# Kernel tuning notes

Hardware: AMD Instinct MI355X
Metric: run time of the kernel (lower is better)

## Reference

```python
import jax, jax.numpy as jnp
import numpy as np

B, H, W = 16, 512, 512
N_BINS = 511          # round(mean(shape)) - 1 for (512, 512)
MAX_R = 1.0           # (1 + min(shape)/max(shape)) / 2 for square image


def _bin_ids():
    # Precompute per-pixel radial shell index (replaces the list of boolean shell masks).
    frame = max(H, W)
    xx, yy = np.mgrid[:H, :W]
    ellipse = ((xx - H / 2) * 2 / frame) ** 2 + ((yy - W / 2) * 2 / frame) ** 2
    r2 = np.linspace(0.0, MAX_R, N_BINS + 1)[1:] ** 2
    # shell k = { r2[k-1] <= ellipse < r2[k] }; pixels with ellipse >= r2[-1] map to
    # overflow bin N_BINS and are dropped, exactly matching the xor'd ellipse masks.
    return jnp.asarray(np.searchsorted(r2, ellipse.ravel(), side='right').astype(np.int32))


BIN_IDS = _bin_ids()  # [H*W] int32 in [0, N_BINS]


def setup_inputs() -> dict:
    key = jax.random.key(0)
    k1, k2 = jax.random.split(key)
    return {
        "z_": jax.random.normal(k1, (B, H, W, 2), dtype=jnp.float32),
        "t_": jax.random.normal(k2, (B, H, W, 2), dtype=jnp.float32),
    }


def _shell_sums(x):
    # x: [B, H*W] -> per-shell sums [B, N_BINS+1] in a single fused segment-sum pass.
    return jax.vmap(lambda v: jax.ops.segment_sum(v, BIN_IDS, num_segments=N_BINS + 1))(x)


def reference(z_, t_):
    tc = t_[..., 0] + 1j * t_[..., 1]          # [B,H,W] complex target
    zc = z_[..., 0] + 1j * z_[..., 1]
    Ft = jnp.fft.fft2(tc, axes=(-2, -1))
    Fe = jnp.fft.fft2(zc - tc, axes=(-2, -1))
    norm_coeff = Ft.real ** 2 + Ft.imag ** 2   # |FFT(target)|^2, [B,H,W]
    errors = Fe.real ** 2 + Fe.imag ** 2       # |FFT(z - target)|^2
    es = _shell_sums(errors.reshape(B, -1))[:, :N_BINS]      # drop overflow bin
    ns = _shell_sums(norm_coeff.reshape(B, -1))[:, :N_BINS]
    nre = es / jnp.maximum(ns, 1e-8)           # per-batch, per-shell normed error
    # per_shell_loss = per-batch sum over shells; loss = mean over batch
    return jnp.mean(jnp.sum(nre, axis=1))
```

## Files before the change

kernel.cpp:

```cpp
#include <hip/hip_runtime.h>

#define HH 512
#define WW 512
#define NBATCH 16
#define NBINS 512

#define PI_F 3.14159265358979323846f

#define SW(r) ((r) ^ (((r) >> 4) & 0xF))
#define TSW(c, hh) (((c) << 3) + ((hh) ^ (((c) >> 1) & 7)))

__device__ __forceinline__ float2 cadd(float2 a, float2 b){ return make_float2(a.x+b.x, a.y+b.y); }
__device__ __forceinline__ float2 csub(float2 a, float2 b){ return make_float2(a.x-b.x, a.y-b.y); }
__device__ __forceinline__ float2 cmul(float2 a, float2 b){
    return make_float2(a.x*b.x - a.y*b.y, a.x*b.y + a.y*b.x);
}

__device__ __forceinline__ void dft8(const float2* a, float2* y) {
    const float s2 = 0.70710678118654752440f;
    float2 t02a = cadd(a[0], a[4]), t02s = csub(a[0], a[4]);
    float2 t13a = cadd(a[2], a[6]), t13s = csub(a[2], a[6]);
    float2 E0 = cadd(t02a, t13a);
    float2 E2 = csub(t02a, t13a);
    float2 E1 = make_float2(t02s.x + t13s.y, t02s.y - t13s.x);
    float2 E3 = make_float2(t02s.x - t13s.y, t02s.y + t13s.x);
    float2 u02a = cadd(a[1], a[5]), u02s = csub(a[1], a[5]);
    float2 u13a = cadd(a[3], a[7]), u13s = csub(a[3], a[7]);
    float2 O0 = cadd(u02a, u13a);
    float2 O2 = csub(u02a, u13a);
    float2 O1 = make_float2(u02s.x + u13s.y, u02s.y - u13s.x);
    float2 O3 = make_float2(u02s.x - u13s.y, u02s.y + u13s.x);
    float2 wO1 = make_float2(s2 * (O1.x + O1.y), s2 * (O1.y - O1.x));
    float2 wO2 = make_float2(O2.y, -O2.x);
    float2 wO3 = make_float2(s2 * (O3.y - O3.x), -s2 * (O3.x + O3.y));
    y[0] = cadd(E0, O0);  y[4] = csub(E0, O0);
    y[1] = cadd(E1, wO1); y[5] = csub(E1, wO1);
    y[2] = cadd(E2, wO2); y[6] = csub(E2, wO2);
    y[3] = cadd(E3, wO3); y[7] = csub(E3, wO3);
}

__device__ __forceinline__ void twiddle8(float base, float2* w) {
    float s1, c1, s4, c4;
    __sincosf(base, &s1, &c1);
    __sincosf(4.0f * base, &s4, &c4);
    w[0] = make_float2(1.0f, 0.0f);
    w[1] = make_float2(c1, s1);
    w[2] = cmul(w[1], w[1]);
    w[3] = cmul(w[2], w[1]);
    w[4] = make_float2(c4, s4);
    w[5] = cmul(w[4], w[1]);
    w[6] = cmul(w[4], w[2]);
    w[7] = cmul(w[4], w[3]);
}

__device__ __forceinline__ void fft512_stage0_store(float2* rb, int lane, const float2* a) {
    float2 y[8]; dft8(a, y);
    float2 w[8]; twiddle8(-PI_F * (float)lane * (1.0f / 256.0f), w);
#pragma unroll
    for (int r = 0; r < 8; ++r) rb[SW(8 * lane + r)] = cmul(y[r], w[r]);
}

__device__ __forceinline__ void fft512_stage1(float2* rb, int lane) {
    float2 a[8];
#pragma unroll
    for (int u = 0; u < 8; ++u) a[u] = rb[SW(lane + 64 * u)];
    float2 y[8]; dft8(a, y);
    float2 w[8]; twiddle8(-PI_F * (float)(lane >> 3) * (1.0f / 32.0f), w);
    const int qb = (lane & 7) + ((lane >> 3) << 6);
#pragma unroll
    for (int r = 0; r < 8; ++r) rb[SW(qb + 8 * r)] = cmul(y[r], w[r]);
}

__device__ __forceinline__ void fft512_stage2(const float2* rb, int lane, float2* y) {
    float2 a[8];
#pragma unroll
    for (int u = 0; u < 8; ++u) a[u] = rb[SW(lane + 64 * u)];
    dft8(a, y);
}

__global__ __launch_bounds__(512, 4)
void row_fft_kernel(const float2* __restrict__ z, const float2* __restrict__ t,
                    float2* __restrict__ fieldsT, int b0) {
    __shared__ float2 buf[8 * 512];
    const int tid  = threadIdx.x;
    const int lane = tid & 63;
    const int g    = tid >> 6;
    const int bid  = blockIdx.x;
    const int hg   = bid & 63;
    const int lb   = bid >> 6;
    const int b    = b0 + lb;
    const int h    = (hg << 3) | g;
    const size_t rowOff = ((size_t)(b * HH + h)) * WW;

    const float2* tr = t + rowOff;
    const float2* zr = z + rowOff;
    float2 tv[8], zv[8];
#pragma unroll
    for (int u = 0; u < 8; ++u) tv[u] = tr[lane + 64 * u];
#pragma unroll
    for (int u = 0; u < 8; ++u) zv[u] = zr[lane + 64 * u];

    float2* rb = buf + (g << 9);
#pragma unroll
    for (int f = 0; f < 2; ++f) {
        float2 a[8];
        if (f == 0) {
#pragma unroll
            for (int u = 0; u < 8; ++u) a[u] = tv[u];
        } else {
#pragma unroll
            for (int u = 0; u < 8; ++u) a[u] = make_float2(zv[u].x - tv[u].x,
                                                           zv[u].y - tv[u].y);
        }
        fft512_stage0_store(rb, lane, a);
        __builtin_amdgcn_wave_barrier();
        fft512_stage1(rb, lane);
        __builtin_amdgcn_wave_barrier();
        float2 y[8];
        fft512_stage2(rb, lane, y);

        __syncthreads();
#pragma unroll
        for (int r = 0; r < 8; ++r) {
            int c = lane + (r << 6);
            buf[TSW(c, g)] = y[r];
        }
        __syncthreads();
        float2* outF = fieldsT + ((size_t)(lb * 2 + f) << 18);
#pragma unroll
        for (int k = 0; k < 8; ++k) {
            int e  = tid + (k << 9);
            int c  = e >> 3;
            int hh = e & 7;
            outF[((size_t)c << 9) + (hg << 3) + hh] = buf[TSW(c, hh)];
        }
        __syncthreads();
    }
}

__global__ __launch_bounds__(512, 4)
void col_fft_bin_kernel(const float2* __restrict__ fieldsT,
                        float* __restrict__ bins, int b0) {
    __shared__ float2 buf[8 * 512];
    __shared__ float hist[NBINS];
    const int tid  = threadIdx.x;
    const int lane = tid & 63;
    const int g    = tid >> 6;
    const int bid  = blockIdx.x;
    const int cg   = bid & 63;
    const int fl   = bid >> 6;
    const int f    = fl & 1;
    const int b    = b0 + (fl >> 1);
    const int c    = (cg << 3) | g;

    hist[tid] = 0.0f;
    __syncthreads();

    const float2* colT = fieldsT + (((size_t)fl << 9) + c) * 512;
    float2 a[8];
#pragma unroll
    for (int u = 0; u < 8; ++u) a[u] = colT[lane + (u << 6)];

    float2* rb = buf + (g << 9);
    fft512_stage0_store(rb, lane, a);
    __builtin_amdgcn_wave_barrier();
    fft512_stage1(rb, lane);
    __builtin_amdgcn_wave_barrier();
    float2 y[8];
    fft512_stage2(rb, lane, y);

    const float fcv = (float)(c - 256) * (1.0f / 256.0f);
    const float fc2 = fcv * fcv;
#pragma unroll
    for (int r = 0; r < 8; ++r) {
        int k = lane + (r << 6);
        float fr = (float)(k - 256) * (1.0f / 256.0f);
        float e = fr * fr + fc2;
        if (e < 1.0f) {
            int bin = (int)(sqrt((double)e) * 511.0);
            atomicAdd(&hist[bin], y[r].x * y[r].x + y[r].y * y[r].y);
        }
    }
    __syncthreads();
    atomicAdd(&bins[((size_t)f * NBATCH + b) * NBINS + tid], hist[tid]);
}

__global__ __launch_bounds__(512)
void loss_kernel(const float* __restrict__ bins, float* __restrict__ outp) {
    __shared__ float red[512];
    const int tid = threadIdx.x;
    float acc = 0.0f;
    if (tid < 511) {
#pragma unroll 4
        for (int b = 0; b < NBATCH; ++b) {
            float ns = bins[((size_t)b) * NBINS + tid];
            float es = bins[((size_t)(NBATCH + b)) * NBINS + tid];
            acc += es / fmaxf(ns, 1e-8f);
        }
    }
    red[tid] = acc;
    __syncthreads();
    for (int s = 256; s > 0; s >>= 1) {
        if (tid < s) red[tid] += red[tid + s];
        __syncthreads();
    }
    if (tid == 0) outp[0] = red[0] * (1.0f / NBATCH);
}

extern "C" void kernel_launch(void* const* d_in, const int* in_sizes, int n_in,
                              void* d_out, int out_size, void* d_ws, size_t ws_size,
                              hipStream_t stream) {
    const float2* z = (const float2*)d_in[0];
    const float2* t = (const float2*)d_in[1];
    float* outp = (float*)d_out;

    const size_t binsBytes = (size_t)2 * NBATCH * NBINS * sizeof(float);
    const size_t fpb = (size_t)2 * HH * WW * sizeof(float2);

    int CB = 16;
    while (CB > 1 && binsBytes + (size_t)CB * fpb > ws_size) CB >>= 1;

    float*  bins    = (float*)d_ws;
    float2* fieldsT = (float2*)((char*)d_ws + binsBytes);

    hipMemsetAsync(bins, 0, binsBytes, stream);

    for (int b0 = 0; b0 < NBATCH; b0 += CB) {
        row_fft_kernel<<<CB * 64, 512, 0, stream>>>(z, t, fieldsT, b0);
        col_fft_bin_kernel<<<CB * 2 * 64, 512, 0, stream>>>(fieldsT, bins, b0);
    }
    loss_kernel<<<1, 512, 0, stream>>>(bins, outp);
}
```

Baseline: 159.6 us.

## Use per-wave LDS histograms and deterministic partials instead of global atomics

The column FFT kernel now reuses each wave's FFT scratch buffer as a private histogram. This removes the shared block histogram's cross-wave atomic contention and the initial zero-fill barrier. The bin index is computed from integer squared radius with a float sqrt plus an exact integer correction, replacing the double-precision sqrt. Per-block partial histograms are written without global atomics and summed by a new reduce kernel, which also drops the memset. In exchange the code adds an extra kernel launch and a 4 MB partials buffer in the workspace.

```diff
diff --git a/kernel.cpp b/kernel.cpp
--- a/kernel.cpp
+++ b/kernel.cpp
@@ -140,9 +140,8 @@
 
 __global__ __launch_bounds__(512, 4)
 void col_fft_bin_kernel(const float2* __restrict__ fieldsT,
-                        float* __restrict__ bins, int b0) {
+                        float* __restrict__ partials, int b0) {
     __shared__ float2 buf[8 * 512];
-    __shared__ float hist[NBINS];
     const int tid  = threadIdx.x;
     const int lane = tid & 63;
     const int g    = tid >> 6;
@@ -153,9 +152,6 @@
     const int b    = b0 + (fl >> 1);
     const int c    = (cg << 3) | g;
 
-    hist[tid] = 0.0f;
-    __syncthreads();
-
     const float2* colT = fieldsT + (((size_t)fl << 9) + c) * 512;
     float2 a[8];
 #pragma unroll
@@ -168,21 +164,60 @@
     __builtin_amdgcn_wave_barrier();
     float2 y[8];
     fft512_stage2(rb, lane, y);
-
-    const float fcv = (float)(c - 256) * (1.0f / 256.0f);
-    const float fc2 = fcv * fcv;
+    __builtin_amdgcn_wave_barrier();
+    __asm__ volatile("" ::: "memory");
+
+#pragma unroll
+    for (int j = 0; j < 4; ++j) rb[lane + (j << 6)] = make_float2(0.0f, 0.0f);
+    __builtin_amdgcn_wave_barrier();
+    __asm__ volatile("" ::: "memory");
+
+    float* histw = (float*)rb;
+    const int dc = c - 256;
+    const unsigned fc2i = (unsigned)(dc * dc);
 #pragma unroll
     for (int r = 0; r < 8; ++r) {
-        int k = lane + (r << 6);
-        float fr = (float)(k - 256) * (1.0f / 256.0f);
-        float e = fr * fr + fc2;
-        if (e < 1.0f) {
-            int bin = (int)(sqrt((double)e) * 511.0);
-            atomicAdd(&hist[bin], y[r].x * y[r].x + y[r].y * y[r].y);
+        int k  = lane + (r << 6);
+        int dk = k - 256;
+        unsigned m = (unsigned)(dk * dk) + fc2i;
+        if (m < 65536u) {
+            int bin = (int)(sqrtf((float)m) * (511.0f / 256.0f));
+            unsigned long long rhs = 261121ull * (unsigned long long)m;
+            unsigned bp1 = (unsigned)(bin + 1);
+            if (((unsigned long long)(bp1 * bp1) << 16) <= rhs) ++bin;
+            else if (((unsigned long long)((unsigned)bin * (unsigned)bin) << 16) > rhs) --bin;
+            atomicAdd(&histw[bin], y[r].x * y[r].x + y[r].y * y[r].y);
         }
     }
     __syncthreads();
-    atomicAdd(&bins[((size_t)f * NBATCH + b) * NBINS + tid], hist[tid]);
+
+    float s = 0.0f;
+    const float* bufF = (const float*)buf;
+#pragma unroll
+    for (int gg = 0; gg < 8; ++gg) s += bufF[(gg << 10) + tid];
+    partials[(((size_t)cg << 5) + (size_t)(f * NBATCH + b)) * NBINS + tid] = s;
+}
+
+__global__ __launch_bounds__(512)
+void reduce_bins_kernel(const float* __restrict__ partials, float* __restrict__ bins) {
+    __shared__ float red[512];
+    const int tid = threadIdx.x;
+    const int fl  = blockIdx.x >> 2;
+    const int q   = blockIdx.x & 3;
+    const int bin = (q << 7) + (tid & 127);
+    const int ch  = tid >> 7;
+    float s = 0.0f;
+#pragma unroll
+    for (int j = 0; j < 16; ++j) {
+        int cg = (ch << 4) + j;
+        s += partials[((size_t)(cg << 5) + fl) * NBINS + bin];
+    }
+    red[tid] = s;
+    __syncthreads();
+    if (tid < 128) {
+        bins[(size_t)fl * NBINS + bin] =
+            red[tid] + red[tid + 128] + red[tid + 256] + red[tid + 384];
+    }
 }
 
 __global__ __launch_bounds__(512)
@@ -214,20 +249,22 @@
     const float2* t = (const float2*)d_in[1];
     float* outp = (float*)d_out;
 
-    const size_t binsBytes = (size_t)2 * NBATCH * NBINS * sizeof(float);
+    const size_t partialsBytes = 64ull * 2 * NBATCH * NBINS * sizeof(float);
+    const size_t binsBytes     = (size_t)2 * NBATCH * NBINS * sizeof(float);
+    const size_t fixedBytes    = partialsBytes + binsBytes;
     const size_t fpb = (size_t)2 * HH * WW * sizeof(float2);
 
     int CB = 16;
-    while (CB > 1 && binsBytes + (size_t)CB * fpb > ws_size) CB >>= 1;
-
-    float*  bins    = (float*)d_ws;
-    float2* fieldsT = (float2*)((char*)d_ws + binsBytes);
-
-    hipMemsetAsync(bins, 0, binsBytes, stream);
+    while (CB > 1 && fixedBytes + (size_t)CB * fpb > ws_size) CB >>= 1;
+
+    float*  partials = (float*)d_ws;
+    float*  bins     = (float*)((char*)d_ws + partialsBytes);
+    float2* fieldsT  = (float2*)((char*)d_ws + fixedBytes);
 
     for (int b0 = 0; b0 < NBATCH; b0 += CB) {
         row_fft_kernel<<<CB * 64, 512, 0, stream>>>(z, t, fieldsT, b0);
-        col_fft_bin_kernel<<<CB * 2 * 64, 512, 0, stream>>>(fieldsT, bins, b0);
-    }
+        col_fft_bin_kernel<<<CB * 2 * 64, 512, 0, stream>>>(fieldsT, partials, b0);
+    }
+    reduce_bins_kernel<<<128, 512, 0, stream>>>(partials, bins);
     loss_kernel<<<1, 512, 0, stream>>>(bins, outp);
 }
```

Result: no change. 161.3 us (+1.1%).
